# Kernel optimization log

Measured on AMD Instinct MI355X. Metric: run time of the kernel, lower is better.

Reference implementation:

```python
import jax, jax.numpy as jnp
import numpy as np

B, T = 64, 1024
ATTN_DIM, RNN_DIM, ENC_DIM = 128, 1024, 512
N_FILT, KSIZE = 32, 31
PAD = (KSIZE - 1) // 2


def setup_inputs() -> dict:
    key = jax.random.key(0)
    ks = jax.random.split(key, 11)
    query = jax.random.normal(ks[0], (B, RNN_DIM), dtype=jnp.float32)
    keys = jax.random.normal(ks[1], (B, T, ENC_DIM), dtype=jnp.float32)
    values = jax.random.normal(ks[2], (B, T, ENC_DIM), dtype=jnp.float32)
    attention_weights_cum = jax.random.uniform(ks[3], (B, T), dtype=jnp.float32)
    mask = jnp.zeros((B, T), dtype=bool)
    s = 0.02
    W_loc_conv = jax.random.normal(ks[4], (N_FILT, 1, KSIZE), dtype=jnp.float32) * s
    W_loc_proj = jax.random.normal(ks[5], (ATTN_DIM, N_FILT), dtype=jnp.float32) * s
    W_query = jax.random.normal(ks[6], (ATTN_DIM, RNN_DIM), dtype=jnp.float32) * s
    W_key = jax.random.normal(ks[7], (ATTN_DIM, ENC_DIM), dtype=jnp.float32) * s
    W_value = jax.random.normal(ks[8], (ENC_DIM, ENC_DIM), dtype=jnp.float32) * s
    W_attn = jax.random.normal(ks[9], (1, ATTN_DIM), dtype=jnp.float32) * s
    return {
        "query": query, "keys": keys, "values": values,
        "attention_weights_cum": attention_weights_cum, "mask": mask,
        "W_loc_conv": W_loc_conv, "W_loc_proj": W_loc_proj,
        "W_query": W_query, "W_key": W_key, "W_value": W_value, "W_attn": W_attn,
    }


def reference(query, keys, values, attention_weights_cum, mask,
              W_loc_conv, W_loc_proj, W_query, W_key, W_value, W_attn):
    # location features: conv1d over cumulative attention, (B,1,T) -> (B,N_FILT,T)
    loc = jax.lax.conv_general_dilated(
        attention_weights_cum[:, None, :], W_loc_conv,
        window_strides=(1,), padding=[(PAD, PAD)],
        dimension_numbers=("NCH", "OIH", "NCH"))
    # (B,T,N_FILT) @ W_loc_proj.T -> (B,T,ATTN_DIM)
    loc_feat = jnp.einsum("bft,af->bta", loc, W_loc_proj)
    q_proj = query @ W_query.T                      # (B, ATTN_DIM)
    k_proj = jnp.einsum("bte,ae->bta", keys, W_key)  # (B, T, ATTN_DIM)
    energies = jnp.tanh(q_proj[:, None, :] + k_proj + loc_feat)
    scores = jnp.einsum("bta,a->bt", energies, W_attn[0])  # (B, T)
    scores = jnp.where(mask, -jnp.inf, scores)
    attn = jax.nn.softmax(scores, axis=-1)
    v_proj = jnp.einsum("bte,fe->btf", values, W_value)  # (B, T, ENC_DIM)
    context = jnp.einsum("bt,btf->bf", attn, v_proj)      # (B, ENC_DIM)
    return context, attn
```

## Files before the change

### kernel.cpp

```cpp
#include <hip/hip_runtime.h>
#include <math.h>

#define B_   64
#define T_   1024
#define AD   128
#define RD   1024
#define ED   512
#define NF   32
#define KS   31
#define PADW 15

#define SA   72
#define SL   40

typedef short bf16x8 __attribute__((ext_vector_type(8)));
typedef float f32x4  __attribute__((ext_vector_type(4)));

__device__ __forceinline__ short f2bf(float x) {
  union { float f; unsigned u; } v; v.f = x;
  unsigned r = (v.u + 0x7FFFu + ((v.u >> 16) & 1u)) >> 16;
  return (short)r;
}

__device__ __forceinline__ float tanh_fast(float x) {
  float t = __expf(2.0f * x);
  return (t - 1.0f) * __builtin_amdgcn_rcpf(t + 1.0f);
}

__global__ __launch_bounds__(256) void prepw_kernel(
    const float* __restrict__ Wk, const float* __restrict__ Wlp,
    short* __restrict__ Wk16, short* __restrict__ Wlp16) {
  int p = blockIdx.x * 256 + threadIdx.x;
  const float* src; short* dst; int off;
  if (p < 16384) { src = Wk; dst = Wk16; off = p; }
  else           { src = Wlp; dst = Wlp16; off = p - 16384; }
  float4 v = *(const float4*)&src[off * 4];
  short4 h = { f2bf(v.x), f2bf(v.y), f2bf(v.z), f2bf(v.w) };
  *(short4*)&dst[off * 4] = h;
}

__global__ __launch_bounds__(256) void conv_kernel(
    const float* __restrict__ awc, const float* __restrict__ Wc,
    short* __restrict__ loc_g) {
  __shared__ float awc_s[128 + KS - 1];
  __shared__ float wc_s[NF * KS];
  const int b = blockIdx.y, t0 = blockIdx.x * 128, tid = threadIdx.x;
  for (int i = tid; i < NF * KS; i += 256) wc_s[i] = Wc[i];
  if (tid < 128 + KS - 1) {
    int gt = t0 - PADW + tid;
    awc_s[tid] = (gt >= 0 && gt < T_) ? awc[b * T_ + gt] : 0.0f;
  }
  __syncthreads();
  const int t = tid & 127, fh = (tid >> 7) * 16;
  for (int fq = 0; fq < 4; ++fq) {
    float s0 = 0.f, s1 = 0.f, s2 = 0.f, s3 = 0.f;
    const float* w0 = &wc_s[(fh + fq * 4 + 0) * KS];
    const float* w1 = &wc_s[(fh + fq * 4 + 1) * KS];
    const float* w2 = &wc_s[(fh + fq * 4 + 2) * KS];
    const float* w3 = &wc_s[(fh + fq * 4 + 3) * KS];
#pragma unroll
    for (int k = 0; k < KS; ++k) {
      float aw = awc_s[t + k];
      s0 += w0[k] * aw; s1 += w1[k] * aw; s2 += w2[k] * aw; s3 += w3[k] * aw;
    }
    short4 h = { f2bf(s0), f2bf(s1), f2bf(s2), f2bf(s3) };
    *(short4*)&loc_g[((size_t)(b * T_ + t0 + t)) * NF + fh + fq * 4] = h;
  }
}

__global__ __launch_bounds__(256) void qproj_kernel(
    const float* __restrict__ query, const float* __restrict__ Wq,
    float* __restrict__ qp) {
  __shared__ float q_s[RD];
  __shared__ float red[AD];
  const int b = blockIdx.x, tid = threadIdx.x;
  *(float4*)&q_s[tid * 4] = *(const float4*)&query[b * RD + tid * 4];
  __syncthreads();
  const int a = tid & 127, kh = tid >> 7;
  const float* wr = &Wq[(size_t)a * RD + kh * 512];
  const float* qr = &q_s[kh * 512];
  float acc = 0.f;
  for (int e = 0; e < 512; e += 4) {
    float4 w = *(const float4*)&wr[e];
    acc += w.x * qr[e] + w.y * qr[e + 1] + w.z * qr[e + 2] + w.w * qr[e + 3];
  }
  if (kh == 1) red[a] = acc;
  __syncthreads();
  if (kh == 0) qp[b * AD + a] = acc + red[a];
}

__global__ __launch_bounds__(256, 3) void scores_kernel(
    const float* __restrict__ keys, const short* __restrict__ Wk16,
    const short* __restrict__ Wlp16, const short* __restrict__ loc_g,
    const float* __restrict__ qp, const float* __restrict__ Wa,
    float* __restrict__ scores) {
  __shared__ alignas(16) short As[128 * SA];
  __shared__ alignas(16) short Bs[128 * SA];
  __shared__ alignas(16) short Ls[128 * SL];
  __shared__ float qp_s[AD], wa_s[AD];
  __shared__ float sc_s[128 * 2];

  const int tid = threadIdx.x;
  const int b = blockIdx.y, t0 = blockIdx.x * 128;
  const int lane = tid & 63, wave = tid >> 6;
  const int wm = wave >> 1, wn = wave & 1;
  const int m16 = lane & 15, s4 = lane >> 4;

  if (tid < AD) { qp_s[tid] = qp[b * AD + tid]; wa_s[tid] = Wa[tid]; }
#pragma unroll
  for (int i = 0; i < 4; ++i) {
    int p = i * 256 + tid, r = p >> 3, c = (p & 7) * 4;
    *(short4*)&Ls[r * SL + c] =
        *(const short4*)&loc_g[((size_t)(b * T_ + t0 + r)) * NF + c];
  }

  f32x4 acc[4][4];
#pragma unroll
  for (int mt = 0; mt < 4; ++mt)
#pragma unroll
    for (int nt = 0; nt < 4; ++nt) acc[mt][nt] = (f32x4){0.f, 0.f, 0.f, 0.f};

  const int arow = wm * 64 + m16, brow = wn * 64 + m16;
  const float* kb = keys + ((size_t)(b * T_ + t0)) * ED;

  for (int kc = 0; kc < 8; ++kc) {
    __syncthreads();
#pragma unroll
    for (int i = 0; i < 8; ++i) {
      int p = i * 256 + tid, e4 = p & 15, r = p >> 4;
      float4 v = *(const float4*)&kb[(size_t)r * ED + kc * 64 + e4 * 4];
      short4 h = { f2bf(v.x), f2bf(v.y), f2bf(v.z), f2bf(v.w) };
      *(short4*)&As[r * SA + e4 * 4] = h;
    }
#pragma unroll
    for (int i = 0; i < 4; ++i) {
      int p = i * 256 + tid, c8 = p & 7, r = p >> 3;
      *(int4*)&Bs[r * SA + c8 * 8] =
          *(const int4*)&Wk16[(size_t)r * ED + kc * 64 + c8 * 8];
    }
    __syncthreads();
#pragma unroll
    for (int kk = 0; kk < 64; kk += 32) {
      bf16x8 af[4], bfr[4];
      const int ko = kk + s4 * 8;
#pragma unroll
      for (int mt = 0; mt < 4; ++mt)
        af[mt] = *(const bf16x8*)&As[(arow + mt * 16) * SA + ko];
#pragma unroll
      for (int nt = 0; nt < 4; ++nt)
        bfr[nt] = *(const bf16x8*)&Bs[(brow + nt * 16) * SA + ko];
#pragma unroll
      for (int mt = 0; mt < 4; ++mt)
#pragma unroll
        for (int nt = 0; nt < 4; ++nt)
          acc[mt][nt] = __builtin_amdgcn_mfma_f32_16x16x32_bf16(
              af[mt], bfr[nt], acc[mt][nt], 0, 0, 0);
    }
  }

  __syncthreads();
#pragma unroll
  for (int i = 0; i < 2; ++i) {
    int p = i * 256 + tid, c = p & 3, r = p >> 2;
    *(int4*)&Bs[r * SA + c * 8] = *(const int4*)&Wlp16[r * NF + c * 8];
  }
  __syncthreads();
  {
    bf16x8 af[4], bfr[4];
#pragma unroll
    for (int mt = 0; mt < 4; ++mt) {
      union { bf16x8 v; short4 h[2]; } u;
      u.h[0] = *(const short4*)&Ls[(arow + mt * 16) * SL + s4 * 8];
      u.h[1] = *(const short4*)&Ls[(arow + mt * 16) * SL + s4 * 8 + 4];
      af[mt] = u.v;
    }
#pragma unroll
    for (int nt = 0; nt < 4; ++nt)
      bfr[nt] = *(const bf16x8*)&Bs[(brow + nt * 16) * SA + s4 * 8];
#pragma unroll
    for (int mt = 0; mt < 4; ++mt)
#pragma unroll
      for (int nt = 0; nt < 4; ++nt)
        acc[mt][nt] = __builtin_amdgcn_mfma_f32_16x16x32_bf16(
            af[mt], bfr[nt], acc[mt][nt], 0, 0, 0);
  }

  float qv[4], wv[4];
#pragma unroll
  for (int nt = 0; nt < 4; ++nt) {
    int a = wn * 64 + nt * 16 + m16;
    qv[nt] = qp_s[a]; wv[nt] = wa_s[a];
  }
#pragma unroll
  for (int mt = 0; mt < 4; ++mt) {
#pragma unroll
    for (int r = 0; r < 4; ++r) {
      float p = 0.f;
#pragma unroll
      for (int nt = 0; nt < 4; ++nt)
        p += wv[nt] * tanh_fast(acc[mt][nt][r] + qv[nt]);
      p += __shfl_xor(p, 1); p += __shfl_xor(p, 2);
      p += __shfl_xor(p, 4); p += __shfl_xor(p, 8);
      if (m16 == 0) sc_s[(wm * 64 + mt * 16 + s4 * 4 + r) * 2 + wn] = p;
    }
  }
  __syncthreads();
  if (tid < 128)
    scores[(size_t)b * T_ + t0 + tid] = sc_s[tid * 2] + sc_s[tid * 2 + 1];
}

__global__ __launch_bounds__(256) void softmax_kernel(
    const float* __restrict__ scores, const unsigned char* __restrict__ mask,
    float* __restrict__ attn) {
  const int b = blockIdx.x, tid = threadIdx.x;
  __shared__ float redm[4], reds[4];

  float4 s4 = *(const float4*)&scores[b * T_ + tid * 4];
  uchar4 m4 = *(const uchar4*)&mask[b * T_ + tid * 4];
  if (m4.x) s4.x = -INFINITY;
  if (m4.y) s4.y = -INFINITY;
  if (m4.z) s4.z = -INFINITY;
  if (m4.w) s4.w = -INFINITY;

  float mx = fmaxf(fmaxf(s4.x, s4.y), fmaxf(s4.z, s4.w));
#pragma unroll
  for (int off = 32; off >= 1; off >>= 1) mx = fmaxf(mx, __shfl_xor(mx, off, 64));
  if ((tid & 63) == 0) redm[tid >> 6] = mx;
  __syncthreads();
  mx = fmaxf(fmaxf(redm[0], redm[1]), fmaxf(redm[2], redm[3]));

  float e0 = expf(s4.x - mx), e1 = expf(s4.y - mx);
  float e2 = expf(s4.z - mx), e3 = expf(s4.w - mx);
  float sum = e0 + e1 + e2 + e3;
#pragma unroll
  for (int off = 32; off >= 1; off >>= 1) sum += __shfl_xor(sum, off, 64);
  if ((tid & 63) == 0) reds[tid >> 6] = sum;
  __syncthreads();
  sum = reds[0] + reds[1] + reds[2] + reds[3];

  float inv = 1.0f / sum;
  float4 o4 = { e0 * inv, e1 * inv, e2 * inv, e3 * inv };
  *(float4*)&attn[b * T_ + tid * 4] = o4;
}

__global__ __launch_bounds__(256) void wvsum_kernel(
    const float* __restrict__ values, const float* __restrict__ attn,
    float* __restrict__ wvp) {
  const int tc = blockIdx.x, b = blockIdx.y, tid = threadIdx.x;
  __shared__ float at_s[32];
  if (tid < 32) at_s[tid] = attn[b * T_ + tc * 32 + tid];
  __syncthreads();
  const int e4 = tid & 127, th = tid >> 7;
  const float* vb = values + ((size_t)(b * T_ + tc * 32 + th * 16)) * ED + e4 * 4;
  float4 acc = {0.f, 0.f, 0.f, 0.f};
#pragma unroll
  for (int t = 0; t < 16; ++t) {
    float a = at_s[th * 16 + t];
    float4 v = *(const float4*)&vb[(size_t)t * ED];
    acc.x = fmaf(a, v.x, acc.x); acc.y = fmaf(a, v.y, acc.y);
    acc.z = fmaf(a, v.z, acc.z); acc.w = fmaf(a, v.w, acc.w);
  }
  *(float4*)&wvp[((size_t)(b * 64 + tc * 2 + th)) * ED + e4 * 4] = acc;
}

__global__ __launch_bounds__(256) void context_kernel(
    const float* __restrict__ wvp, const float* __restrict__ Wv,
    float* __restrict__ ctx) {
  const int fq = blockIdx.x, b = blockIdx.y, tid = threadIdx.x;
  __shared__ float wv_s[ED];
  __shared__ float red[128];
  for (int e = tid; e < ED; e += 256) {
    float s = 0.f;
    const float* base = &wvp[(size_t)b * 64 * ED + e];
#pragma unroll
    for (int p = 0; p < 64; ++p) s += base[p * ED];
    wv_s[e] = s;
  }
  __syncthreads();
  const int fl = tid & 127, eh = tid >> 7;
  const int f = fq * 128 + fl;
  const float* wr = &Wv[(size_t)f * ED + eh * 256];
  const float* qr = &wv_s[eh * 256];
  float acc = 0.f;
  for (int e = 0; e < 256; e += 4) {
    float4 w = *(const float4*)&wr[e];
    acc += w.x * qr[e] + w.y * qr[e + 1] + w.z * qr[e + 2] + w.w * qr[e + 3];
  }
  if (eh == 1) red[fl] = acc;
  __syncthreads();
  if (eh == 0) ctx[b * ED + f] = acc + red[fl];
}

extern "C" void kernel_launch(void* const* d_in, const int* in_sizes, int n_in,
                              void* d_out, int out_size, void* d_ws, size_t ws_size,
                              hipStream_t stream) {
  const float* query = (const float*)d_in[0];
  const float* keys  = (const float*)d_in[1];
  const float* values= (const float*)d_in[2];
  const float* awc   = (const float*)d_in[3];
  const unsigned char* mask = (const unsigned char*)d_in[4];
  const float* Wc    = (const float*)d_in[5];
  const float* Wlp   = (const float*)d_in[6];
  const float* Wq    = (const float*)d_in[7];
  const float* Wk    = (const float*)d_in[8];
  const float* Wv    = (const float*)d_in[9];
  const float* Wa    = (const float*)d_in[10];

  float* ctx  = (float*)d_out;
  float* attn = (float*)d_out + B_ * ED;

  float* ws = (float*)d_ws;
  float* qp      = ws;
  float* scoresB = qp + B_ * AD;
  float* wvp     = scoresB + B_ * T_;
  short* Wk16    = (short*)(wvp + (size_t)B_ * 64 * ED);
  short* Wlp16   = Wk16 + AD * ED;
  short* loc_g   = Wlp16 + AD * NF;

  prepw_kernel<<<68, 256, 0, stream>>>(Wk, Wlp, Wk16, Wlp16);
  conv_kernel<<<dim3(8, 64), 256, 0, stream>>>(awc, Wc, loc_g);
  qproj_kernel<<<B_, 256, 0, stream>>>(query, Wq, qp);
  scores_kernel<<<dim3(8, 64), 256, 0, stream>>>(keys, Wk16, Wlp16, loc_g, qp, Wa, scoresB);
  softmax_kernel<<<B_, 256, 0, stream>>>(scoresB, mask, attn);
  wvsum_kernel<<<dim3(32, B_), 256, 0, stream>>>(values, attn, wvp);
  context_kernel<<<dim3(4, B_), 256, 0, stream>>>(wvp, Wv, ctx);
}
```

Baseline: 360.1 us.

## Merge prep kernels, retile scores GEMM with register prefetch, coarsen wvsum

Folds the weight-conversion, location-conv and query-projection kernels into one launch, with each block range picking its role. The scores kernel now uses 64-row tiles (1024 blocks) in which each wave owns 32 attention columns. It prefetches the next key chunk and Wk16 chunk into registers while the MFMAs run, and drops the occupancy hint in launch bounds. The wvsum kernel handles 64 timesteps per block, which halves the partial buffer that the context kernel reduces. The aim is fewer launches, more parallel blocks and global load latency hidden behind compute, at the cost of more register pressure and more rereads of Wk16 across blocks.

New measurement: 360.4 us. Within noise of the previous version (+0.1%).

```diff
diff --git a/kernel.cpp b/kernel.cpp
--- a/kernel.cpp
+++ b/kernel.cpp
@@ -27,132 +27,158 @@
   return (t - 1.0f) * __builtin_amdgcn_rcpf(t + 1.0f);
 }
 
-__global__ __launch_bounds__(256) void prepw_kernel(
+__global__ __launch_bounds__(256) void prep_kernel(
     const float* __restrict__ Wk, const float* __restrict__ Wlp,
-    short* __restrict__ Wk16, short* __restrict__ Wlp16) {
-  int p = blockIdx.x * 256 + threadIdx.x;
-  const float* src; short* dst; int off;
-  if (p < 16384) { src = Wk; dst = Wk16; off = p; }
-  else           { src = Wlp; dst = Wlp16; off = p - 16384; }
-  float4 v = *(const float4*)&src[off * 4];
-  short4 h = { f2bf(v.x), f2bf(v.y), f2bf(v.z), f2bf(v.w) };
-  *(short4*)&dst[off * 4] = h;
-}
-
-__global__ __launch_bounds__(256) void conv_kernel(
     const float* __restrict__ awc, const float* __restrict__ Wc,
-    short* __restrict__ loc_g) {
-  __shared__ float awc_s[128 + KS - 1];
-  __shared__ float wc_s[NF * KS];
-  const int b = blockIdx.y, t0 = blockIdx.x * 128, tid = threadIdx.x;
-  for (int i = tid; i < NF * KS; i += 256) wc_s[i] = Wc[i];
-  if (tid < 128 + KS - 1) {
-    int gt = t0 - PADW + tid;
-    awc_s[tid] = (gt >= 0 && gt < T_) ? awc[b * T_ + gt] : 0.0f;
-  }
-  __syncthreads();
-  const int t = tid & 127, fh = (tid >> 7) * 16;
-  for (int fq = 0; fq < 4; ++fq) {
-    float s0 = 0.f, s1 = 0.f, s2 = 0.f, s3 = 0.f;
-    const float* w0 = &wc_s[(fh + fq * 4 + 0) * KS];
-    const float* w1 = &wc_s[(fh + fq * 4 + 1) * KS];
-    const float* w2 = &wc_s[(fh + fq * 4 + 2) * KS];
-    const float* w3 = &wc_s[(fh + fq * 4 + 3) * KS];
-#pragma unroll
-    for (int k = 0; k < KS; ++k) {
-      float aw = awc_s[t + k];
-      s0 += w0[k] * aw; s1 += w1[k] * aw; s2 += w2[k] * aw; s3 += w3[k] * aw;
-    }
-    short4 h = { f2bf(s0), f2bf(s1), f2bf(s2), f2bf(s3) };
-    *(short4*)&loc_g[((size_t)(b * T_ + t0 + t)) * NF + fh + fq * 4] = h;
-  }
-}
-
-__global__ __launch_bounds__(256) void qproj_kernel(
     const float* __restrict__ query, const float* __restrict__ Wq,
-    float* __restrict__ qp) {
-  __shared__ float q_s[RD];
-  __shared__ float red[AD];
-  const int b = blockIdx.x, tid = threadIdx.x;
-  *(float4*)&q_s[tid * 4] = *(const float4*)&query[b * RD + tid * 4];
-  __syncthreads();
-  const int a = tid & 127, kh = tid >> 7;
-  const float* wr = &Wq[(size_t)a * RD + kh * 512];
-  const float* qr = &q_s[kh * 512];
-  float acc = 0.f;
-  for (int e = 0; e < 512; e += 4) {
-    float4 w = *(const float4*)&wr[e];
-    acc += w.x * qr[e] + w.y * qr[e + 1] + w.z * qr[e + 2] + w.w * qr[e + 3];
-  }
-  if (kh == 1) red[a] = acc;
-  __syncthreads();
-  if (kh == 0) qp[b * AD + a] = acc + red[a];
-}
-
-__global__ __launch_bounds__(256, 3) void scores_kernel(
+    short* __restrict__ Wk16, short* __restrict__ Wlp16,
+    short* __restrict__ loc_g, float* __restrict__ qp) {
+  __shared__ float sh_awc[128 + KS - 1];
+  __shared__ float sh_wc[NF * KS];
+  __shared__ float sh_q[RD];
+  __shared__ float sh_red[AD];
+  const int blk = blockIdx.x, tid = threadIdx.x;
+
+  if (blk < 68) {
+    int p = blk * 256 + tid;
+    const float* src; short* dst; int off;
+    if (p < 16384) { src = Wk; dst = Wk16; off = p; }
+    else           { src = Wlp; dst = Wlp16; off = p - 16384; }
+    float4 v = *(const float4*)&src[off * 4];
+    short4 h = { f2bf(v.x), f2bf(v.y), f2bf(v.z), f2bf(v.w) };
+    *(short4*)&dst[off * 4] = h;
+  } else if (blk < 580) {
+    int cb = blk - 68;
+    int b = cb >> 3, t0 = (cb & 7) * 128;
+    for (int i = tid; i < NF * KS; i += 256) sh_wc[i] = Wc[i];
+    if (tid < 128 + KS - 1) {
+      int gt = t0 - PADW + tid;
+      sh_awc[tid] = (gt >= 0 && gt < T_) ? awc[b * T_ + gt] : 0.0f;
+    }
+    __syncthreads();
+    const int t = tid & 127, fh = (tid >> 7) * 16;
+    for (int fq = 0; fq < 4; ++fq) {
+      float s0 = 0.f, s1 = 0.f, s2 = 0.f, s3 = 0.f;
+      const float* w0 = &sh_wc[(fh + fq * 4 + 0) * KS];
+      const float* w1 = &sh_wc[(fh + fq * 4 + 1) * KS];
+      const float* w2 = &sh_wc[(fh + fq * 4 + 2) * KS];
+      const float* w3 = &sh_wc[(fh + fq * 4 + 3) * KS];
+#pragma unroll
+      for (int k = 0; k < KS; ++k) {
+        float aw = sh_awc[t + k];
+        s0 += w0[k] * aw; s1 += w1[k] * aw; s2 += w2[k] * aw; s3 += w3[k] * aw;
+      }
+      short4 h = { f2bf(s0), f2bf(s1), f2bf(s2), f2bf(s3) };
+      *(short4*)&loc_g[((size_t)(b * T_ + t0 + t)) * NF + fh + fq * 4] = h;
+    }
+  } else {
+    int b = blk - 580;
+    *(float4*)&sh_q[tid * 4] = *(const float4*)&query[b * RD + tid * 4];
+    __syncthreads();
+    const int a = tid & 127, kh = tid >> 7;
+    const float* wr = &Wq[(size_t)a * RD + kh * 512];
+    const float* qr = &sh_q[kh * 512];
+    float acc = 0.f;
+    for (int e = 0; e < 512; e += 4) {
+      float4 w = *(const float4*)&wr[e];
+      acc += w.x * qr[e] + w.y * qr[e + 1] + w.z * qr[e + 2] + w.w * qr[e + 3];
+    }
+    if (kh == 1) sh_red[a] = acc;
+    __syncthreads();
+    if (kh == 0) qp[b * AD + a] = acc + sh_red[a];
+  }
+}
+
+__global__ __launch_bounds__(256) void scores_kernel(
     const float* __restrict__ keys, const short* __restrict__ Wk16,
     const short* __restrict__ Wlp16, const short* __restrict__ loc_g,
     const float* __restrict__ qp, const float* __restrict__ Wa,
     float* __restrict__ scores) {
-  __shared__ alignas(16) short As[128 * SA];
+  __shared__ alignas(16) short As[64 * SA];
   __shared__ alignas(16) short Bs[128 * SA];
-  __shared__ alignas(16) short Ls[128 * SL];
+  __shared__ alignas(16) short Ls[64 * SL];
   __shared__ float qp_s[AD], wa_s[AD];
-  __shared__ float sc_s[128 * 2];
+  __shared__ float sc_s[64 * 4];
 
   const int tid = threadIdx.x;
-  const int b = blockIdx.y, t0 = blockIdx.x * 128;
+  const int b = blockIdx.y, t0 = blockIdx.x * 64;
   const int lane = tid & 63, wave = tid >> 6;
-  const int wm = wave >> 1, wn = wave & 1;
   const int m16 = lane & 15, s4 = lane >> 4;
 
   if (tid < AD) { qp_s[tid] = qp[b * AD + tid]; wa_s[tid] = Wa[tid]; }
+  {
+    int r = tid >> 2, c = tid & 3;
+    *(int4*)&Ls[r * SL + c * 8] =
+        *(const int4*)&loc_g[((size_t)(b * T_ + t0 + r)) * NF + c * 8];
+  }
+
+  f32x4 acc[4][2];
+#pragma unroll
+  for (int mt = 0; mt < 4; ++mt)
+#pragma unroll
+    for (int nt = 0; nt < 2; ++nt) acc[mt][nt] = (f32x4){0.f, 0.f, 0.f, 0.f};
+
+  const float* kb = keys + ((size_t)(b * T_ + t0)) * ED;
+  float4 pa[4]; int4 pb[4]; int4 pw[2];
+
 #pragma unroll
   for (int i = 0; i < 4; ++i) {
-    int p = i * 256 + tid, r = p >> 3, c = (p & 7) * 4;
-    *(short4*)&Ls[r * SL + c] =
-        *(const short4*)&loc_g[((size_t)(b * T_ + t0 + r)) * NF + c];
-  }
-
-  f32x4 acc[4][4];
-#pragma unroll
-  for (int mt = 0; mt < 4; ++mt)
-#pragma unroll
-    for (int nt = 0; nt < 4; ++nt) acc[mt][nt] = (f32x4){0.f, 0.f, 0.f, 0.f};
-
-  const int arow = wm * 64 + m16, brow = wn * 64 + m16;
-  const float* kb = keys + ((size_t)(b * T_ + t0)) * ED;
+    int p = i * 256 + tid;
+    pa[i] = *(const float4*)&kb[(size_t)(p >> 4) * ED + (p & 15) * 4];
+  }
+#pragma unroll
+  for (int i = 0; i < 4; ++i) {
+    int p = i * 256 + tid;
+    pb[i] = *(const int4*)&Wk16[(size_t)(p >> 3) * ED + (p & 7) * 8];
+  }
 
   for (int kc = 0; kc < 8; ++kc) {
     __syncthreads();
 #pragma unroll
-    for (int i = 0; i < 8; ++i) {
-      int p = i * 256 + tid, e4 = p & 15, r = p >> 4;
-      float4 v = *(const float4*)&kb[(size_t)r * ED + kc * 64 + e4 * 4];
-      short4 h = { f2bf(v.x), f2bf(v.y), f2bf(v.z), f2bf(v.w) };
+    for (int i = 0; i < 4; ++i) {
+      int p = i * 256 + tid, r = p >> 4, e4 = p & 15;
+      short4 h = { f2bf(pa[i].x), f2bf(pa[i].y), f2bf(pa[i].z), f2bf(pa[i].w) };
       *(short4*)&As[r * SA + e4 * 4] = h;
     }
 #pragma unroll
     for (int i = 0; i < 4; ++i) {
-      int p = i * 256 + tid, c8 = p & 7, r = p >> 3;
-      *(int4*)&Bs[r * SA + c8 * 8] =
-          *(const int4*)&Wk16[(size_t)r * ED + kc * 64 + c8 * 8];
-    }
-    __syncthreads();
+      int p = i * 256 + tid, r = p >> 3, c8 = p & 7;
+      *(int4*)&Bs[r * SA + c8 * 8] = pb[i];
+    }
+    __syncthreads();
+    if (kc < 7) {
+      int ko = (kc + 1) * 64;
+#pragma unroll
+      for (int i = 0; i < 4; ++i) {
+        int p = i * 256 + tid;
+        pa[i] = *(const float4*)&kb[(size_t)(p >> 4) * ED + ko + (p & 15) * 4];
+      }
+#pragma unroll
+      for (int i = 0; i < 4; ++i) {
+        int p = i * 256 + tid;
+        pb[i] = *(const int4*)&Wk16[(size_t)(p >> 3) * ED + ko + (p & 7) * 8];
+      }
+    } else {
+#pragma unroll
+      for (int i = 0; i < 2; ++i) {
+        int p = i * 256 + tid;
+        pw[i] = *(const int4*)&Wlp16[(p >> 2) * NF + (p & 3) * 8];
+      }
+    }
 #pragma unroll
     for (int kk = 0; kk < 64; kk += 32) {
-      bf16x8 af[4], bfr[4];
       const int ko = kk + s4 * 8;
+      bf16x8 af[4], bfr[2];
 #pragma unroll
       for (int mt = 0; mt < 4; ++mt)
-        af[mt] = *(const bf16x8*)&As[(arow + mt * 16) * SA + ko];
-#pragma unroll
-      for (int nt = 0; nt < 4; ++nt)
-        bfr[nt] = *(const bf16x8*)&Bs[(brow + nt * 16) * SA + ko];
+        af[mt] = *(const bf16x8*)&As[(mt * 16 + m16) * SA + ko];
+#pragma unroll
+      for (int nt = 0; nt < 2; ++nt)
+        bfr[nt] = *(const bf16x8*)&Bs[(wave * 32 + nt * 16 + m16) * SA + ko];
 #pragma unroll
       for (int mt = 0; mt < 4; ++mt)
 #pragma unroll
-        for (int nt = 0; nt < 4; ++nt)
+        for (int nt = 0; nt < 2; ++nt)
           acc[mt][nt] = __builtin_amdgcn_mfma_f32_16x16x32_bf16(
               af[mt], bfr[nt], acc[mt][nt], 0, 0, 0);
     }
@@ -161,52 +187,49 @@
   __syncthreads();
 #pragma unroll
   for (int i = 0; i < 2; ++i) {
-    int p = i * 256 + tid, c = p & 3, r = p >> 2;
-    *(int4*)&Bs[r * SA + c * 8] = *(const int4*)&Wlp16[r * NF + c * 8];
+    int p = i * 256 + tid;
+    *(int4*)&Bs[(p >> 2) * SA + (p & 3) * 8] = pw[i];
   }
   __syncthreads();
   {
-    bf16x8 af[4], bfr[4];
-#pragma unroll
-    for (int mt = 0; mt < 4; ++mt) {
-      union { bf16x8 v; short4 h[2]; } u;
-      u.h[0] = *(const short4*)&Ls[(arow + mt * 16) * SL + s4 * 8];
-      u.h[1] = *(const short4*)&Ls[(arow + mt * 16) * SL + s4 * 8 + 4];
-      af[mt] = u.v;
-    }
-#pragma unroll
-    for (int nt = 0; nt < 4; ++nt)
-      bfr[nt] = *(const bf16x8*)&Bs[(brow + nt * 16) * SA + s4 * 8];
+    const int ko = s4 * 8;
+    bf16x8 af[4], bfr[2];
 #pragma unroll
     for (int mt = 0; mt < 4; ++mt)
-#pragma unroll
-      for (int nt = 0; nt < 4; ++nt)
+      af[mt] = *(const bf16x8*)&Ls[(mt * 16 + m16) * SL + ko];
+#pragma unroll
+    for (int nt = 0; nt < 2; ++nt)
+      bfr[nt] = *(const bf16x8*)&Bs[(wave * 32 + nt * 16 + m16) * SA + ko];
+#pragma unroll
+    for (int mt = 0; mt < 4; ++mt)
+#pragma unroll
+      for (int nt = 0; nt < 2; ++nt)
         acc[mt][nt] = __builtin_amdgcn_mfma_f32_16x16x32_bf16(
             af[mt], bfr[nt], acc[mt][nt], 0, 0, 0);
   }
 
-  float qv[4], wv[4];
-#pragma unroll
-  for (int nt = 0; nt < 4; ++nt) {
-    int a = wn * 64 + nt * 16 + m16;
+  float qv[2], wv[2];
+#pragma unroll
+  for (int nt = 0; nt < 2; ++nt) {
+    int a = wave * 32 + nt * 16 + m16;
     qv[nt] = qp_s[a]; wv[nt] = wa_s[a];
   }
 #pragma unroll
   for (int mt = 0; mt < 4; ++mt) {
 #pragma unroll
     for (int r = 0; r < 4; ++r) {
-      float p = 0.f;
-#pragma unroll
-      for (int nt = 0; nt < 4; ++nt)
-        p += wv[nt] * tanh_fast(acc[mt][nt][r] + qv[nt]);
+      float p = wv[0] * tanh_fast(acc[mt][0][r] + qv[0]) +
+                wv[1] * tanh_fast(acc[mt][1][r] + qv[1]);
       p += __shfl_xor(p, 1); p += __shfl_xor(p, 2);
       p += __shfl_xor(p, 4); p += __shfl_xor(p, 8);
-      if (m16 == 0) sc_s[(wm * 64 + mt * 16 + s4 * 4 + r) * 2 + wn] = p;
-    }
-  }
-  __syncthreads();
-  if (tid < 128)
-    scores[(size_t)b * T_ + t0 + tid] = sc_s[tid * 2] + sc_s[tid * 2 + 1];
+      if (m16 == 0) sc_s[(mt * 16 + s4 * 4 + r) * 4 + wave] = p;
+    }
+  }
+  __syncthreads();
+  if (tid < 64) {
+    float4 v = *(const float4*)&sc_s[tid * 4];
+    scores[(size_t)b * T_ + t0 + tid] = v.x + v.y + v.z + v.w;
+  }
 }
 
 __global__ __launch_bounds__(256) void softmax_kernel(
@@ -247,20 +270,21 @@
     const float* __restrict__ values, const float* __restrict__ attn,
     float* __restrict__ wvp) {
   const int tc = blockIdx.x, b = blockIdx.y, tid = threadIdx.x;
-  __shared__ float at_s[32];
-  if (tid < 32) at_s[tid] = attn[b * T_ + tc * 32 + tid];
+  __shared__ float at_s[64];
+  if (tid < 64) at_s[tid] = attn[b * T_ + tc * 64 + tid];
   __syncthreads();
   const int e4 = tid & 127, th = tid >> 7;
-  const float* vb = values + ((size_t)(b * T_ + tc * 32 + th * 16)) * ED + e4 * 4;
+  const float* vb =
+      values + ((size_t)(b * T_ + tc * 64 + th * 32)) * ED + e4 * 4;
   float4 acc = {0.f, 0.f, 0.f, 0.f};
-#pragma unroll
-  for (int t = 0; t < 16; ++t) {
-    float a = at_s[th * 16 + t];
+#pragma unroll 8
+  for (int t = 0; t < 32; ++t) {
+    float a = at_s[th * 32 + t];
     float4 v = *(const float4*)&vb[(size_t)t * ED];
     acc.x = fmaf(a, v.x, acc.x); acc.y = fmaf(a, v.y, acc.y);
     acc.z = fmaf(a, v.z, acc.z); acc.w = fmaf(a, v.w, acc.w);
   }
-  *(float4*)&wvp[((size_t)(b * 64 + tc * 2 + th)) * ED + e4 * 4] = acc;
+  *(float4*)&wvp[((size_t)(b * 32 + tc * 2 + th)) * ED + e4 * 4] = acc;
 }
 
 __global__ __launch_bounds__(256) void context_kernel(
@@ -271,9 +295,9 @@
   __shared__ float red[128];
   for (int e = tid; e < ED; e += 256) {
     float s = 0.f;
-    const float* base = &wvp[(size_t)b * 64 * ED + e];
-#pragma unroll
-    for (int p = 0; p < 64; ++p) s += base[p * ED];
+    const float* base = &wvp[(size_t)b * 32 * ED + e];
+#pragma unroll
+    for (int p = 0; p < 32; ++p) s += base[p * ED];
     wv_s[e] = s;
   }
   __syncthreads();
@@ -313,15 +337,15 @@
   float* qp      = ws;
   float* scoresB = qp + B_ * AD;
   float* wvp     = scoresB + B_ * T_;
-  short* Wk16    = (short*)(wvp + (size_t)B_ * 64 * ED);
+  short* Wk16    = (short*)(wvp + (size_t)B_ * 32 * ED);
   short* Wlp16   = Wk16 + AD * ED;
   short* loc_g   = Wlp16 + AD * NF;
 
-  prepw_kernel<<<68, 256, 0, stream>>>(Wk, Wlp, Wk16, Wlp16);
-  conv_kernel<<<dim3(8, 64), 256, 0, stream>>>(awc, Wc, loc_g);
-  qproj_kernel<<<B_, 256, 0, stream>>>(query, Wq, qp);
-  scores_kernel<<<dim3(8, 64), 256, 0, stream>>>(keys, Wk16, Wlp16, loc_g, qp, Wa, scoresB);
+  prep_kernel<<<644, 256, 0, stream>>>(Wk, Wlp, awc, Wc, query, Wq,
+                                       Wk16, Wlp16, loc_g, qp);
+  scores_kernel<<<dim3(16, B_), 256, 0, stream>>>(keys, Wk16, Wlp16, loc_g,
+                                                  qp, Wa, scoresB);
   softmax_kernel<<<B_, 256, 0, stream>>>(scoresB, mask, attn);
-  wvsum_kernel<<<dim3(32, B_), 256, 0, stream>>>(values, attn, wvp);
+  wvsum_kernel<<<dim3(16, B_), 256, 0, stream>>>(values, attn, wvp);
   context_kernel<<<dim3(4, B_), 256, 0, stream>>>(wvp, Wv, ctx);
 }
```
